# Kernel optimization log

Measured on AMD Instinct MI355X. Metric: run time of the kernel, lower is better.

The kernel has to match this reference:

```python
import jax, jax.numpy as jnp
import numpy as np

B, P, D = 8192, 1024, 256  # batch, nprototypes (32x32 map), latent_dim


def setup_inputs() -> dict:
    key = jax.random.key(0)
    k1, k2 = jax.random.split(key)
    inputs = jax.random.normal(k1, (B, D), dtype=jnp.float32)
    # glorot-uniform-style init for prototypes
    limit = np.sqrt(6.0 / (P + D)).astype(np.float32)
    prototypes = jax.random.uniform(k2, (P, D), dtype=jnp.float32, minval=-limit, maxval=limit)
    return {"inputs": inputs, "prototypes": prototypes}


def reference(inputs, prototypes):
    # Faithful to: mean_p( sum_d (x[b,d] - proto[p,d])^2 )
    # computed in fused cdist form to avoid the (B,P,D) broadcast tensor:
    x2 = jnp.sum(inputs * inputs, axis=-1)          # (B,)
    p2 = jnp.sum(prototypes * prototypes, axis=-1)  # (P,)
    cross = jnp.einsum('bd,pd->bp', inputs, prototypes)  # (B,P)
    dist = x2[:, None] + p2[None, :] - 2.0 * cross  # (B,P) squared distances
    return jnp.mean(dist, axis=-1)                  # (B,) mean over prototypes
```

## Files before the change

### kernel.cpp

```cpp
#include <hip/hip_runtime.h>
#include <hip/hip_bf16.h>


#define SOM_B 8192
#define SOM_P 1024
#define SOM_D 256
#define NPART 16

__global__ __launch_bounds__(256) void som_proto_partial(
    const float* __restrict__ proto, float* __restrict__ ws) {
    const int lane = threadIdx.x & 63;
    const int wv   = threadIdx.x >> 6;
    const int row0 = blockIdx.x * 64 + wv * 16;
    const float4* p4 = (const float4*)proto;

    float4 cs = {0.f, 0.f, 0.f, 0.f};
    float sq = 0.f;
#pragma unroll
    for (int i = 0; i < 16; ++i) {
        float4 v = p4[(size_t)(row0 + i) * (SOM_D / 4) + lane];
        cs.x += v.x; cs.y += v.y; cs.z += v.z; cs.w += v.w;
        sq   += v.x * v.x + v.y * v.y + v.z * v.z + v.w * v.w;
    }
    __shared__ float4 lds_cs[4][64];
    __shared__ float  lds_sq[4];
#pragma unroll
    for (int off = 32; off; off >>= 1) sq += __shfl_down(sq, off, 64);
    if (lane == 0) lds_sq[wv] = sq;
    lds_cs[wv][lane] = cs;
    __syncthreads();
    if (threadIdx.x < 64) {
        float4 a = lds_cs[0][lane], b = lds_cs[1][lane];
        float4 c = lds_cs[2][lane], d = lds_cs[3][lane];
        float4 t;
        t.x = (a.x + b.x) + (c.x + d.x);
        t.y = (a.y + b.y) + (c.y + d.y);
        t.z = (a.z + b.z) + (c.z + d.z);
        t.w = (a.w + b.w) + (c.w + d.w);
        ((float4*)(ws + (size_t)blockIdx.x * SOM_D))[lane] = t;
        if (lane == 0)
            ws[NPART * SOM_D + blockIdx.x] =
                (lds_sq[0] + lds_sq[1]) + (lds_sq[2] + lds_sq[3]);
    }
}

__global__ __launch_bounds__(256) void som_out_kernel(
    const float* __restrict__ x, const float* __restrict__ ws,
    float* __restrict__ out) {
    __shared__ float4 cs4[SOM_D / 4];
    __shared__ float  sqp_lds;
    const int t = threadIdx.x;

    float c = 0.f;
#pragma unroll
    for (int g = 0; g < NPART; ++g) c += ws[g * SOM_D + t];
    ((float*)cs4)[t] = c;
    if (t == 0) {
        float s = 0.f;
#pragma unroll
        for (int g = 0; g < NPART; ++g) s += ws[NPART * SOM_D + g];
        sqp_lds = s;
    }
    __syncthreads();

    const int lane = t & 63;
    const int wv   = t >> 6;
    const int row  = blockIdx.x * 4 + wv;

    const float4 xv = ((const float4*)(x + (size_t)row * SOM_D))[lane];
    const float4 mv = cs4[lane];

    float sq = xv.x * xv.x + xv.y * xv.y + xv.z * xv.z + xv.w * xv.w;
    float dt = xv.x * mv.x + xv.y * mv.y + xv.z * mv.z + xv.w * mv.w;
#pragma unroll
    for (int off = 32; off; off >>= 1) {
        sq += __shfl_down(sq, off, 64);
        dt += __shfl_down(dt, off, 64);
    }
    if (lane == 0) {
        const float invP = 1.0f / (float)SOM_P;
        out[row] = sq + (sqp_lds - 2.0f * dt) * invP;
    }
}

extern "C" void kernel_launch(void* const* d_in, const int* in_sizes, int n_in,
                              void* d_out, int out_size, void* d_ws, size_t ws_size,
                              hipStream_t stream) {
    const float* x     = (const float*)d_in[0];
    const float* proto = (const float*)d_in[1];
    float* out = (float*)d_out;
    float* ws  = (float*)d_ws;

    som_proto_partial<<<NPART, 256, 0, stream>>>(proto, ws);
    som_out_kernel<<<SOM_B / 4, 256, 0, stream>>>(x, ws, out);
}
```

Baseline: 62.85 us.

## Widen prototype reduction split and process four rows per wave in output kernel

Doubles the number of prototype partial-sum blocks (32 blocks of 32 rows) so the first kernel spreads across more CUs. The output kernel now handles 16 rows per block, four per wave, so the per-block reduction of the workspace partials is amortised over four times as many rows and far fewer blocks re-read it. Workspace traffic goes through relaxed agent-scope atomic loads and stores, and the prototype squared-norm sum is reduced with a wave shuffle. The atomics may add per-element access cost, and the larger per-wave work lowers the block count.

```diff
diff --git a/kernel.cpp b/kernel.cpp
--- a/kernel.cpp
+++ b/kernel.cpp
@@ -5,19 +5,26 @@
 #define SOM_B 8192
 #define SOM_P 1024
 #define SOM_D 256
-#define NPART 16
+#define NPART 32
+
+__device__ __forceinline__ void ws_store(float* p, float v) {
+    __hip_atomic_store(p, v, __ATOMIC_RELAXED, __HIP_MEMORY_SCOPE_AGENT);
+}
+__device__ __forceinline__ float ws_load(const float* p) {
+    return __hip_atomic_load(p, __ATOMIC_RELAXED, __HIP_MEMORY_SCOPE_AGENT);
+}
 
 __global__ __launch_bounds__(256) void som_proto_partial(
     const float* __restrict__ proto, float* __restrict__ ws) {
     const int lane = threadIdx.x & 63;
     const int wv   = threadIdx.x >> 6;
-    const int row0 = blockIdx.x * 64 + wv * 16;
+    const int row0 = blockIdx.x * 32 + wv * 8;
     const float4* p4 = (const float4*)proto;
 
     float4 cs = {0.f, 0.f, 0.f, 0.f};
     float sq = 0.f;
 #pragma unroll
-    for (int i = 0; i < 16; ++i) {
+    for (int i = 0; i < 8; ++i) {
         float4 v = p4[(size_t)(row0 + i) * (SOM_D / 4) + lane];
         cs.x += v.x; cs.y += v.y; cs.z += v.z; cs.w += v.w;
         sq   += v.x * v.x + v.y * v.y + v.z * v.z + v.w * v.w;
@@ -32,54 +39,65 @@
     if (threadIdx.x < 64) {
         float4 a = lds_cs[0][lane], b = lds_cs[1][lane];
         float4 c = lds_cs[2][lane], d = lds_cs[3][lane];
-        float4 t;
-        t.x = (a.x + b.x) + (c.x + d.x);
-        t.y = (a.y + b.y) + (c.y + d.y);
-        t.z = (a.z + b.z) + (c.z + d.z);
-        t.w = (a.w + b.w) + (c.w + d.w);
-        ((float4*)(ws + (size_t)blockIdx.x * SOM_D))[lane] = t;
+        float* base = ws + (size_t)blockIdx.x * SOM_D + lane * 4;
+        ws_store(base + 0, (a.x + b.x) + (c.x + d.x));
+        ws_store(base + 1, (a.y + b.y) + (c.y + d.y));
+        ws_store(base + 2, (a.z + b.z) + (c.z + d.z));
+        ws_store(base + 3, (a.w + b.w) + (c.w + d.w));
         if (lane == 0)
-            ws[NPART * SOM_D + blockIdx.x] =
-                (lds_sq[0] + lds_sq[1]) + (lds_sq[2] + lds_sq[3]);
+            ws_store(&ws[NPART * SOM_D + blockIdx.x],
+                     (lds_sq[0] + lds_sq[1]) + (lds_sq[2] + lds_sq[3]));
     }
 }
 
 __global__ __launch_bounds__(256) void som_out_kernel(
     const float* __restrict__ x, const float* __restrict__ ws,
     float* __restrict__ out) {
-    __shared__ float4 cs4[SOM_D / 4];
-    __shared__ float  sqp_lds;
-    const int t = threadIdx.x;
+    __shared__ float cs[SOM_D];
+    __shared__ float sqp_lds;
+    const int t    = threadIdx.x;
+    const int lane = t & 63;
+    const int wv   = t >> 6;
 
-    float c = 0.f;
+    {
+        float c = 0.f;
 #pragma unroll
-    for (int g = 0; g < NPART; ++g) c += ws[g * SOM_D + t];
-    ((float*)cs4)[t] = c;
-    if (t == 0) {
-        float s = 0.f;
+        for (int g = 0; g < NPART; ++g) c += ws_load(&ws[g * SOM_D + t]);
+        cs[t] = c;
+    }
+    if (t < 32) {
+        float s = ws_load(&ws[NPART * SOM_D + t]);
 #pragma unroll
-        for (int g = 0; g < NPART; ++g) s += ws[NPART * SOM_D + g];
-        sqp_lds = s;
+        for (int off = 16; off; off >>= 1) s += __shfl_down(s, off, 32);
+        if (t == 0) sqp_lds = s;
     }
     __syncthreads();
 
-    const int lane = t & 63;
-    const int wv   = t >> 6;
-    const int row  = blockIdx.x * 4 + wv;
+    const float  sqp = sqp_lds;
+    const float4 mv  = ((const float4*)cs)[lane];
+    const int    row0 = blockIdx.x * 16 + wv * 4;
+    const float4* x4  = (const float4*)x;
 
-    const float4 xv = ((const float4*)(x + (size_t)row * SOM_D))[lane];
-    const float4 mv = cs4[lane];
-
-    float sq = xv.x * xv.x + xv.y * xv.y + xv.z * xv.z + xv.w * xv.w;
-    float dt = xv.x * mv.x + xv.y * mv.y + xv.z * mv.z + xv.w * mv.w;
+    float sq[4], dt[4];
 #pragma unroll
-    for (int off = 32; off; off >>= 1) {
-        sq += __shfl_down(sq, off, 64);
-        dt += __shfl_down(dt, off, 64);
+    for (int i = 0; i < 4; ++i) {
+        float4 xv = x4[(size_t)(row0 + i) * 64 + lane];
+        sq[i] = xv.x * xv.x + xv.y * xv.y + xv.z * xv.z + xv.w * xv.w;
+        dt[i] = xv.x * mv.x + xv.y * mv.y + xv.z * mv.z + xv.w * mv.w;
+    }
+#pragma unroll
+    for (int i = 0; i < 4; ++i) {
+#pragma unroll
+        for (int off = 32; off; off >>= 1) {
+            sq[i] += __shfl_down(sq[i], off, 64);
+            dt[i] += __shfl_down(dt[i], off, 64);
+        }
     }
     if (lane == 0) {
         const float invP = 1.0f / (float)SOM_P;
-        out[row] = sq + (sqp_lds - 2.0f * dt) * invP;
+#pragma unroll
+        for (int i = 0; i < 4; ++i)
+            out[row0 + i] = sq[i] + (sqp - 2.0f * dt[i]) * invP;
     }
 }
 
@@ -92,5 +110,5 @@
     float* ws  = (float*)d_ws;
 
     som_proto_partial<<<NPART, 256, 0, stream>>>(proto, ws);
-    som_out_kernel<<<SOM_B / 4, 256, 0, stream>>>(x, ws, out);
+    som_out_kernel<<<SOM_B / 16, 256, 0, stream>>>(x, ws, out);
 }
```

Result: no change. 62.88 us (median of 2 runs) (+0.1%).
